# Performance work log

Hardware: AMD Instinct MI355X
Metric: run time of the kernel (lower is better)

## Reference

```python
import jax, jax.numpy as jnp
import numpy as np

C, C_LO, C_MF = 96, 32, 32  # c_hf = 96 - 32 - 32 = 32
K_LO, K_HI, LP_FINE, LP_COARSE = 5, 3, 3, 7
BN_EPS = 1e-5


def _avgpool_same(x, k):
    """AvgPool2d(k, stride=1, padding=k//2, count_include_pad=False) on NCHW."""
    p = k // 2
    dims, strides = (1, 1, k, k), (1, 1, 1, 1)
    pads = ((0, 0), (0, 0), (p, p), (p, p))
    s = jax.lax.reduce_window(x, jnp.float32(0), jax.lax.add, dims, strides, pads)
    ones = jnp.ones((1, 1) + x.shape[2:], x.dtype)
    cnt = jax.lax.reduce_window(ones, jnp.float32(0), jax.lax.add, dims, strides, pads)
    return s / cnt  # divide by number of VALID (non-pad) elements


def _dwconv(x, w, k):
    """Depthwise conv, 'same' padding, no bias. w: (C, 1, k, k)."""
    p = k // 2
    return jax.lax.conv_general_dilated(
        x, w, window_strides=(1, 1), padding=((p, p), (p, p)),
        dimension_numbers=("NCHW", "OIHW", "NCHW"),
        feature_group_count=x.shape[1])


def setup_inputs() -> dict:
    key = jax.random.key(0)
    ks = jax.random.split(key, 8)
    B, H, W = 8, 256, 256
    return {
        "x": jax.random.normal(ks[0], (B, C, H, W), jnp.float32),
        "w_lo": jax.random.normal(ks[1], (C_LO, 1, K_LO, K_LO), jnp.float32) * 0.1,
        "w_mf": jax.random.normal(ks[2], (C_MF, 1, 3, 3), jnp.float32) * 0.2,
        "w_hf": jax.random.normal(ks[3], (C - C_LO - C_MF, 1, K_HI, K_HI), jnp.float32) * 0.2,
        "bn_gamma": jax.random.uniform(ks[4], (C,), jnp.float32, 0.5, 1.5),
        "bn_beta": jax.random.normal(ks[5], (C,), jnp.float32) * 0.1,
        "bn_mean": jax.random.normal(ks[6], (C,), jnp.float32) * 0.1,
        "bn_var": jax.random.uniform(ks[7], (C,), jnp.float32, 0.5, 1.5),
    }


def reference(x, w_lo, w_mf, w_hf, bn_gamma, bn_beta, bn_mean, bn_var):
    x_lo = x[:, :C_LO]
    x_mf = x[:, C_LO:C_LO + C_MF]
    x_hf = x[:, C_LO + C_MF:]

    y_lo = _dwconv(x_lo, w_lo, K_LO)
    # band-pass: fine low-pass minus coarse low-pass
    x_mf_bp = _avgpool_same(x_mf, LP_FINE) - _avgpool_same(x_mf, LP_COARSE)
    y_mf = _dwconv(x_mf_bp, w_mf, 3)
    # high-pass: identity minus fine low-pass
    x_hf_hp = x_hf - _avgpool_same(x_hf, LP_FINE)
    y_hf = _dwconv(x_hf_hp, w_hf, K_HI)

    y = jnp.concatenate([y_lo, y_mf, y_hf], axis=1)

    # channel shuffle with groups=3 (C % 3 == 0 here)
    B, Cc, H, W = y.shape
    y = y.reshape(B, 3, Cc // 3, H, W).transpose(0, 2, 1, 3, 4).reshape(B, Cc, H, W)

    # BatchNorm2d (inference mode, running stats) + SiLU
    inv = bn_gamma * jax.lax.rsqrt(bn_var + BN_EPS)
    y = y * inv[None, :, None, None] + (bn_beta - bn_mean * inv)[None, :, None, None]
    return jax.nn.silu(y)
```

## Files before the change

kernel.cpp:

```cpp
#include <hip/hip_runtime.h>

#define HH 256
#define WW 256
#define CC 96
#define BB 8

__device__ __forceinline__ float silu_of(float z) {
    return z / (1.0f + __expf(-z));
}

__global__ __launch_bounds__(256, 4)
void trifreq_kernel(const float* __restrict__ x,
                    const float* __restrict__ w_lo,
                    const float* __restrict__ w_mf,
                    const float* __restrict__ w_hf,
                    const float* __restrict__ gamma,
                    const float* __restrict__ beta,
                    const float* __restrict__ mean,
                    const float* __restrict__ var,
                    float* __restrict__ out)
{
    __shared__ float xs[72 * 72];
    __shared__ float tmp[68 * 68];

    const int tid = threadIdx.x;
    const int tileIdx = blockIdx.x;
    const int c = blockIdx.y;
    const int b = blockIdx.z;
    const int th = (tileIdx >> 2) * 64;
    const int tw = (tileIdx & 3) * 64;

    const int g = c >> 5;
    const int ci = c & 31;
    const int c_out = ci * 3 + g;

    const float* __restrict__ xin = x + (((size_t)b * CC + c) * (size_t)HH) * (size_t)WW;

    for (int idx = tid; idx < 72 * 18; idx += 256) {
        const int r  = idx / 18;
        const int c4 = idx % 18;
        const int gh = th - 4 + r;
        const int gw = tw - 4 + 4 * c4;
        float4 v = make_float4(0.f, 0.f, 0.f, 0.f);
        if (gh >= 0 && gh < HH && gw >= 0 && gw + 3 < WW) {
            v = *reinterpret_cast<const float4*>(xin + (size_t)gh * WW + gw);
        }
        *reinterpret_cast<float4*>(&xs[r * 72 + 4 * c4]) = v;
    }
    __syncthreads();

    const int qr = (tid >> 4) << 2;
    const int qc = (tid & 15) << 2;
    float acc[4][4];

    if (g == 0) {
        const float* __restrict__ wp = w_lo + ci * 25;
        float wk[25];
        #pragma unroll
        for (int t = 0; t < 25; ++t) wk[t] = wp[t];
        #pragma unroll
        for (int i = 0; i < 4; ++i)
            #pragma unroll
            for (int j = 0; j < 4; ++j) acc[i][j] = 0.f;

        #pragma unroll
        for (int rr = 0; rr < 8; ++rr) {
            const float* row = &xs[(qr + rr + 2) * 72 + (qc + 2)];
            float v[8];
            #pragma unroll
            for (int j = 0; j < 8; ++j) v[j] = row[j];
            #pragma unroll
            for (int i = 0; i < 4; ++i) {
                const int ki = rr - i;
                if (ki >= 0 && ki < 5) {
                    #pragma unroll
                    for (int j = 0; j < 4; ++j)
                        acc[i][j] += v[j + 0] * wk[ki * 5 + 0]
                                   + v[j + 1] * wk[ki * 5 + 1]
                                   + v[j + 2] * wk[ki * 5 + 2]
                                   + v[j + 3] * wk[ki * 5 + 3]
                                   + v[j + 4] * wk[ki * 5 + 4];
                }
            }
        }
    } else {
        if (g == 1) {
            for (int p = tid; p < 17 * 17; p += 256) {
                const int pr = p / 17, pc = p % 17;
                const int br = pr * 4 - 2, bc = pc * 4 - 2;
                float v7a[4][4] = {};
                float v3a[4][4] = {};
                #pragma unroll
                for (int rr = 0; rr < 10; ++rr) {
                    int xr = br - 3 + rr + 4;
                    xr = max(0, min(71, xr));
                    const float* row = &xs[xr * 72];
                    float v[10];
                    #pragma unroll
                    for (int j = 0; j < 10; ++j) {
                        int xc = bc - 3 + j + 4;
                        xc = max(0, min(71, xc));
                        v[j] = row[xc];
                    }
                    float h7[4], h3[4];
                    float s = v[0] + v[1] + v[2] + v[3] + v[4] + v[5] + v[6];
                    h7[0] = s;
                    h7[1] = h7[0] + v[7] - v[0];
                    h7[2] = h7[1] + v[8] - v[1];
                    h7[3] = h7[2] + v[9] - v[2];
                    #pragma unroll
                    for (int j = 0; j < 4; ++j) h3[j] = v[j + 2] + v[j + 3] + v[j + 4];
                    #pragma unroll
                    for (int k = 0; k < 4; ++k) {
                        if (rr >= k && rr <= k + 6) {
                            #pragma unroll
                            for (int j = 0; j < 4; ++j) v7a[k][j] += h7[j];
                        }
                        if (rr >= k + 2 && rr <= k + 4) {
                            #pragma unroll
                            for (int j = 0; j < 4; ++j) v3a[k][j] += h3[j];
                        }
                    }
                }
                float r3h[4], r7h[4], r3w[4], r7w[4];
                #pragma unroll
                for (int i = 0; i < 4; ++i) {
                    const int hh = th + br + i;
                    const int a3 = min(hh + 1, HH - 1) - max(hh - 1, 0) + 1;
                    const int a7 = min(hh + 3, HH - 1) - max(hh - 3, 0) + 1;
                    r3h[i] = 1.0f / (float)a3;
                    r7h[i] = 1.0f / (float)a7;
                }
                #pragma unroll
                for (int j = 0; j < 4; ++j) {
                    const int ww = tw + bc + j;
                    const int a3 = min(ww + 1, WW - 1) - max(ww - 1, 0) + 1;
                    const int a7 = min(ww + 3, WW - 1) - max(ww - 3, 0) + 1;
                    r3w[j] = 1.0f / (float)a3;
                    r7w[j] = 1.0f / (float)a7;
                }
                #pragma unroll
                for (int i = 0; i < 4; ++i) {
                    const int hh = th + br + i;
                    #pragma unroll
                    for (int j = 0; j < 4; ++j) {
                        const int ww = tw + bc + j;
                        float bp = 0.f;
                        if (hh >= 0 && hh < HH && ww >= 0 && ww < WW)
                            bp = v3a[i][j] * (r3h[i] * r3w[j]) - v7a[i][j] * (r7h[i] * r7w[j]);
                        tmp[(br + i + 2) * 68 + (bc + j + 2)] = bp;
                    }
                }
            }
        } else {
            for (int p = tid; p < 17 * 17; p += 256) {
                const int pr = p / 17, pc = p % 17;
                const int br = pr * 4 - 2, bc = pc * 4 - 2;
                float v3a[4][4] = {};
                float cen[4][4];
                #pragma unroll
                for (int rr = 0; rr < 6; ++rr) {
                    const int xr = br - 1 + rr + 4;
                    const float* row = &xs[xr * 72];
                    float v[6];
                    #pragma unroll
                    for (int j = 0; j < 6; ++j) v[j] = row[bc - 1 + j + 4];
                    float h3[4];
                    #pragma unroll
                    for (int j = 0; j < 4; ++j) h3[j] = v[j] + v[j + 1] + v[j + 2];
                    if (rr >= 1 && rr <= 4) {
                        #pragma unroll
                        for (int j = 0; j < 4; ++j) cen[rr - 1][j] = v[j + 1];
                    }
                    #pragma unroll
                    for (int k = 0; k < 4; ++k) {
                        if (rr >= k && rr <= k + 2) {
                            #pragma unroll
                            for (int j = 0; j < 4; ++j) v3a[k][j] += h3[j];
                        }
                    }
                }
                float r3h[4], r3w[4];
                #pragma unroll
                for (int i = 0; i < 4; ++i) {
                    const int hh = th + br + i;
                    const int a3 = min(hh + 1, HH - 1) - max(hh - 1, 0) + 1;
                    r3h[i] = 1.0f / (float)a3;
                }
                #pragma unroll
                for (int j = 0; j < 4; ++j) {
                    const int ww = tw + bc + j;
                    const int a3 = min(ww + 1, WW - 1) - max(ww - 1, 0) + 1;
                    r3w[j] = 1.0f / (float)a3;
                }
                #pragma unroll
                for (int i = 0; i < 4; ++i) {
                    const int hh = th + br + i;
                    #pragma unroll
                    for (int j = 0; j < 4; ++j) {
                        const int ww = tw + bc + j;
                        float hp = 0.f;
                        if (hh >= 0 && hh < HH && ww >= 0 && ww < WW)
                            hp = cen[i][j] - v3a[i][j] * (r3h[i] * r3w[j]);
                        tmp[(br + i + 2) * 68 + (bc + j + 2)] = hp;
                    }
                }
            }
        }
        __syncthreads();

        const float* __restrict__ wp = ((g == 1) ? w_mf : w_hf) + ci * 9;
        float wk[9];
        #pragma unroll
        for (int t = 0; t < 9; ++t) wk[t] = wp[t];
        #pragma unroll
        for (int i = 0; i < 4; ++i)
            #pragma unroll
            for (int j = 0; j < 4; ++j) acc[i][j] = 0.f;

        #pragma unroll
        for (int rr = 0; rr < 6; ++rr) {
            const float* row = &tmp[(qr + rr + 1) * 68 + (qc + 1)];
            float v[6];
            #pragma unroll
            for (int j = 0; j < 6; ++j) v[j] = row[j];
            #pragma unroll
            for (int i = 0; i < 4; ++i) {
                const int ki = rr - i;
                if (ki >= 0 && ki < 3) {
                    #pragma unroll
                    for (int j = 0; j < 4; ++j)
                        acc[i][j] += v[j + 0] * wk[ki * 3 + 0]
                                   + v[j + 1] * wk[ki * 3 + 1]
                                   + v[j + 2] * wk[ki * 3 + 2];
                }
            }
        }
    }

    const float bninv  = gamma[c_out] * rsqrtf(var[c_out] + 1e-5f);
    const float bnbias = beta[c_out] - mean[c_out] * bninv;
    float* __restrict__ op = out + (((size_t)b * CC + c_out) * (size_t)HH + (th + qr)) * (size_t)WW + (tw + qc);
    #pragma unroll
    for (int i = 0; i < 4; ++i) {
        float4 o;
        const float z0 = acc[i][0] * bninv + bnbias;
        const float z1 = acc[i][1] * bninv + bnbias;
        const float z2 = acc[i][2] * bninv + bnbias;
        const float z3 = acc[i][3] * bninv + bnbias;
        o.x = silu_of(z0);
        o.y = silu_of(z1);
        o.z = silu_of(z2);
        o.w = silu_of(z3);
        *reinterpret_cast<float4*>(op + (size_t)i * WW) = o;
    }
}

extern "C" void kernel_launch(void* const* d_in, const int* in_sizes, int n_in,
                              void* d_out, int out_size, void* d_ws, size_t ws_size,
                              hipStream_t stream) {
    const float* x     = (const float*)d_in[0];
    const float* w_lo  = (const float*)d_in[1];
    const float* w_mf  = (const float*)d_in[2];
    const float* w_hf  = (const float*)d_in[3];
    const float* gam   = (const float*)d_in[4];
    const float* bet   = (const float*)d_in[5];
    const float* mea   = (const float*)d_in[6];
    const float* va    = (const float*)d_in[7];
    float* out = (float*)d_out;

    dim3 grid(16, CC, BB);
    dim3 block(256);
    hipLaunchKernelGGL(trifreq_kernel, grid, block, 0, stream,
                       x, w_lo, w_mf, w_hf, gam, bet, mea, va, out);
}
```

Measured before the change: 390.3 us.

## Use separable shared-memory box filters with smaller 32x64 tiles and precomputed reciprocals

Splits the avgpool filters into a horizontal running-sum pass stored in shared memory, followed by a vertical float4 sum pass. This replaces the per-thread 4x4 recomputation with clamped indexing. Tiles shrink to 32x64, doubling the grid and giving each thread a 2x4 output block. Valid-count reciprocals are precomputed once per block into a small table. This trades more halo overhead and extra barriers for less redundant ALU work, and the higher block count should help occupancy.

Result: no change. 393.4 us (+0.8%).

```diff
diff --git a/kernel.cpp b/kernel.cpp
--- a/kernel.cpp
+++ b/kernel.cpp
@@ -4,6 +4,13 @@
 #define WW 256
 #define CC 96
 #define BB 8
+
+#define TLH 32
+#define TLW 64
+#define XSH 40
+#define XSW 72
+#define HSH 40
+#define HSW 68
 
 __device__ __forceinline__ float silu_of(float z) {
     return z / (1.0f + __expf(-z));
@@ -20,38 +27,49 @@
                     const float* __restrict__ var,
                     float* __restrict__ out)
 {
-    __shared__ float xs[72 * 72];
-    __shared__ float tmp[68 * 68];
+    __shared__ __align__(16) float xs[XSH * XSW];
+    __shared__ __align__(16) float hsA[HSH * HSW];
+    __shared__ __align__(16) float hs7[HSH * HSW];
+    __shared__ float rc[4 * HSW];
 
     const int tid = threadIdx.x;
     const int tileIdx = blockIdx.x;
     const int c = blockIdx.y;
     const int b = blockIdx.z;
-    const int th = (tileIdx >> 2) * 64;
-    const int tw = (tileIdx & 3) * 64;
-
-    const int g = c >> 5;
+    const int th = (tileIdx >> 2) * TLH;
+    const int tw = (tileIdx & 3) * TLW;
+
+    const int g  = c >> 5;
     const int ci = c & 31;
     const int c_out = ci * 3 + g;
 
-    const float* __restrict__ xin = x + (((size_t)b * CC + c) * (size_t)HH) * (size_t)WW;
-
-    for (int idx = tid; idx < 72 * 18; idx += 256) {
+    const float* __restrict__ xin = x + (size_t)(b * CC + c) * (size_t)(HH * WW);
+
+    for (int i = tid; i < 4 * HSW; i += 256) {
+        const int tbl = i / HSW;
+        const int k   = i - tbl * HSW;
+        const int pos = ((tbl < 2) ? th : tw) + (k - 1);
+        const int rad = (tbl & 1) ? 3 : 1;
+        const int cnt = min(pos + rad, HH - 1) - max(pos - rad, 0) + 1;
+        rc[i] = (pos >= 0 && pos < HH) ? (1.0f / (float)cnt) : 0.0f;
+    }
+
+    for (int idx = tid; idx < XSH * 18; idx += 256) {
         const int r  = idx / 18;
-        const int c4 = idx % 18;
+        const int c4 = (idx - r * 18) * 4;
         const int gh = th - 4 + r;
-        const int gw = tw - 4 + 4 * c4;
+        const int gw = tw - 4 + c4;
         float4 v = make_float4(0.f, 0.f, 0.f, 0.f);
-        if (gh >= 0 && gh < HH && gw >= 0 && gw + 3 < WW) {
+        if ((unsigned)gh < (unsigned)HH && (unsigned)gw <= (unsigned)(WW - 4))
             v = *reinterpret_cast<const float4*>(xin + (size_t)gh * WW + gw);
-        }
-        *reinterpret_cast<float4*>(&xs[r * 72 + 4 * c4]) = v;
+        *reinterpret_cast<float4*>(&xs[r * XSW + c4]) = v;
     }
     __syncthreads();
 
-    const int qr = (tid >> 4) << 2;
-    const int qc = (tid & 15) << 2;
-    float acc[4][4];
+    const int qr = (tid >> 4) * 2;
+    const int qc = (tid & 15) * 4;
+    float acc0[4] = {0.f, 0.f, 0.f, 0.f};
+    float acc1[4] = {0.f, 0.f, 0.f, 0.f};
 
     if (g == 0) {
         const float* __restrict__ wp = w_lo + ci * 25;
@@ -59,152 +77,97 @@
         #pragma unroll
         for (int t = 0; t < 25; ++t) wk[t] = wp[t];
         #pragma unroll
-        for (int i = 0; i < 4; ++i)
-            #pragma unroll
-            for (int j = 0; j < 4; ++j) acc[i][j] = 0.f;
-
-        #pragma unroll
-        for (int rr = 0; rr < 8; ++rr) {
-            const float* row = &xs[(qr + rr + 2) * 72 + (qc + 2)];
+        for (int rr = 0; rr < 6; ++rr) {
+            const float* row = &xs[(qr + rr + 2) * XSW + (qc + 2)];
             float v[8];
             #pragma unroll
             for (int j = 0; j < 8; ++j) v[j] = row[j];
-            #pragma unroll
-            for (int i = 0; i < 4; ++i) {
-                const int ki = rr - i;
-                if (ki >= 0 && ki < 5) {
-                    #pragma unroll
-                    for (int j = 0; j < 4; ++j)
-                        acc[i][j] += v[j + 0] * wk[ki * 5 + 0]
-                                   + v[j + 1] * wk[ki * 5 + 1]
-                                   + v[j + 2] * wk[ki * 5 + 2]
-                                   + v[j + 3] * wk[ki * 5 + 3]
-                                   + v[j + 4] * wk[ki * 5 + 4];
+            if (rr < 5) {
+                const float* wr = &wk[rr * 5];
+                #pragma unroll
+                for (int j = 0; j < 4; ++j)
+                    acc0[j] += v[j]*wr[0] + v[j+1]*wr[1] + v[j+2]*wr[2] + v[j+3]*wr[3] + v[j+4]*wr[4];
+            }
+            if (rr >= 1) {
+                const float* wr = &wk[(rr - 1) * 5];
+                #pragma unroll
+                for (int j = 0; j < 4; ++j)
+                    acc1[j] += v[j]*wr[0] + v[j+1]*wr[1] + v[j+2]*wr[2] + v[j+3]*wr[3] + v[j+4]*wr[4];
+            }
+        }
+    } else {
+        for (int t = tid; t < HSH * 11; t += 256) {
+            const int r   = t / 11;
+            const int ci0 = (t - r * 11) * 6;
+            const float* row = &xs[r * XSW + ci0];
+            float v[12];
+            #pragma unroll
+            for (int j = 0; j < 12; ++j) v[j] = row[j];
+            float s7 = v[0]+v[1]+v[2]+v[3]+v[4]+v[5]+v[6];
+            float s3 = v[2]+v[3]+v[4];
+            float* p7 = &hs7[r * HSW + ci0];
+            float* p3 = &hsA[r * HSW + ci0];
+            #pragma unroll
+            for (int j = 0; j < 6; ++j) {
+                p7[j] = s7;
+                p3[j] = s3;
+                if (j < 5) { s7 += v[j+7] - v[j]; s3 += v[j+5] - v[j+2]; }
+            }
+        }
+        __syncthreads();
+
+        float res[3][4];
+        if (g == 1) {
+            int nt = 0;
+            for (int t = tid; t < 34 * 17; t += 256, ++nt) {
+                const int r   = t / 17;
+                const int ci0 = (t - r * 17) * 4;
+                float a7x=0.f, a7y=0.f, a7z=0.f, a7w=0.f;
+                #pragma unroll
+                for (int d = 0; d < 7; ++d) {
+                    const float4 h = *reinterpret_cast<const float4*>(&hs7[(r + d) * HSW + ci0]);
+                    a7x += h.x; a7y += h.y; a7z += h.z; a7w += h.w;
                 }
-            }
-        }
-    } else {
-        if (g == 1) {
-            for (int p = tid; p < 17 * 17; p += 256) {
-                const int pr = p / 17, pc = p % 17;
-                const int br = pr * 4 - 2, bc = pc * 4 - 2;
-                float v7a[4][4] = {};
-                float v3a[4][4] = {};
-                #pragma unroll
-                for (int rr = 0; rr < 10; ++rr) {
-                    int xr = br - 3 + rr + 4;
-                    xr = max(0, min(71, xr));
-                    const float* row = &xs[xr * 72];
-                    float v[10];
-                    #pragma unroll
-                    for (int j = 0; j < 10; ++j) {
-                        int xc = bc - 3 + j + 4;
-                        xc = max(0, min(71, xc));
-                        v[j] = row[xc];
-                    }
-                    float h7[4], h3[4];
-                    float s = v[0] + v[1] + v[2] + v[3] + v[4] + v[5] + v[6];
-                    h7[0] = s;
-                    h7[1] = h7[0] + v[7] - v[0];
-                    h7[2] = h7[1] + v[8] - v[1];
-                    h7[3] = h7[2] + v[9] - v[2];
-                    #pragma unroll
-                    for (int j = 0; j < 4; ++j) h3[j] = v[j + 2] + v[j + 3] + v[j + 4];
-                    #pragma unroll
-                    for (int k = 0; k < 4; ++k) {
-                        if (rr >= k && rr <= k + 6) {
-                            #pragma unroll
-                            for (int j = 0; j < 4; ++j) v7a[k][j] += h7[j];
-                        }
-                        if (rr >= k + 2 && rr <= k + 4) {
-                            #pragma unroll
-                            for (int j = 0; j < 4; ++j) v3a[k][j] += h3[j];
-                        }
-                    }
+                float a3x=0.f, a3y=0.f, a3z=0.f, a3w=0.f;
+                #pragma unroll
+                for (int d = 2; d < 5; ++d) {
+                    const float4 h = *reinterpret_cast<const float4*>(&hsA[(r + d) * HSW + ci0]);
+                    a3x += h.x; a3y += h.y; a3z += h.z; a3w += h.w;
                 }
-                float r3h[4], r7h[4], r3w[4], r7w[4];
-                #pragma unroll
-                for (int i = 0; i < 4; ++i) {
-                    const int hh = th + br + i;
-                    const int a3 = min(hh + 1, HH - 1) - max(hh - 1, 0) + 1;
-                    const int a7 = min(hh + 3, HH - 1) - max(hh - 3, 0) + 1;
-                    r3h[i] = 1.0f / (float)a3;
-                    r7h[i] = 1.0f / (float)a7;
+                const float f3 = rc[r];
+                const float f7 = rc[HSW + r];
+                res[nt][0] = a3x * (f3 * rc[2*HSW + ci0 + 0]) - a7x * (f7 * rc[3*HSW + ci0 + 0]);
+                res[nt][1] = a3y * (f3 * rc[2*HSW + ci0 + 1]) - a7y * (f7 * rc[3*HSW + ci0 + 1]);
+                res[nt][2] = a3z * (f3 * rc[2*HSW + ci0 + 2]) - a7z * (f7 * rc[3*HSW + ci0 + 2]);
+                res[nt][3] = a3w * (f3 * rc[2*HSW + ci0 + 3]) - a7w * (f7 * rc[3*HSW + ci0 + 3]);
+            }
+        } else {
+            int nt = 0;
+            for (int t = tid; t < 34 * 17; t += 256, ++nt) {
+                const int r   = t / 17;
+                const int ci0 = (t - r * 17) * 4;
+                float a3x=0.f, a3y=0.f, a3z=0.f, a3w=0.f;
+                #pragma unroll
+                for (int d = 2; d < 5; ++d) {
+                    const float4 h = *reinterpret_cast<const float4*>(&hsA[(r + d) * HSW + ci0]);
+                    a3x += h.x; a3y += h.y; a3z += h.z; a3w += h.w;
                 }
-                #pragma unroll
-                for (int j = 0; j < 4; ++j) {
-                    const int ww = tw + bc + j;
-                    const int a3 = min(ww + 1, WW - 1) - max(ww - 1, 0) + 1;
-                    const int a7 = min(ww + 3, WW - 1) - max(ww - 3, 0) + 1;
-                    r3w[j] = 1.0f / (float)a3;
-                    r7w[j] = 1.0f / (float)a7;
-                }
-                #pragma unroll
-                for (int i = 0; i < 4; ++i) {
-                    const int hh = th + br + i;
-                    #pragma unroll
-                    for (int j = 0; j < 4; ++j) {
-                        const int ww = tw + bc + j;
-                        float bp = 0.f;
-                        if (hh >= 0 && hh < HH && ww >= 0 && ww < WW)
-                            bp = v3a[i][j] * (r3h[i] * r3w[j]) - v7a[i][j] * (r7h[i] * r7w[j]);
-                        tmp[(br + i + 2) * 68 + (bc + j + 2)] = bp;
-                    }
-                }
-            }
-        } else {
-            for (int p = tid; p < 17 * 17; p += 256) {
-                const int pr = p / 17, pc = p % 17;
-                const int br = pr * 4 - 2, bc = pc * 4 - 2;
-                float v3a[4][4] = {};
-                float cen[4][4];
-                #pragma unroll
-                for (int rr = 0; rr < 6; ++rr) {
-                    const int xr = br - 1 + rr + 4;
-                    const float* row = &xs[xr * 72];
-                    float v[6];
-                    #pragma unroll
-                    for (int j = 0; j < 6; ++j) v[j] = row[bc - 1 + j + 4];
-                    float h3[4];
-                    #pragma unroll
-                    for (int j = 0; j < 4; ++j) h3[j] = v[j] + v[j + 1] + v[j + 2];
-                    if (rr >= 1 && rr <= 4) {
-                        #pragma unroll
-                        for (int j = 0; j < 4; ++j) cen[rr - 1][j] = v[j + 1];
-                    }
-                    #pragma unroll
-                    for (int k = 0; k < 4; ++k) {
-                        if (rr >= k && rr <= k + 2) {
-                            #pragma unroll
-                            for (int j = 0; j < 4; ++j) v3a[k][j] += h3[j];
-                        }
-                    }
-                }
-                float r3h[4], r3w[4];
-                #pragma unroll
-                for (int i = 0; i < 4; ++i) {
-                    const int hh = th + br + i;
-                    const int a3 = min(hh + 1, HH - 1) - max(hh - 1, 0) + 1;
-                    r3h[i] = 1.0f / (float)a3;
-                }
-                #pragma unroll
-                for (int j = 0; j < 4; ++j) {
-                    const int ww = tw + bc + j;
-                    const int a3 = min(ww + 1, WW - 1) - max(ww - 1, 0) + 1;
-                    r3w[j] = 1.0f / (float)a3;
-                }
-                #pragma unroll
-                for (int i = 0; i < 4; ++i) {
-                    const int hh = th + br + i;
-                    #pragma unroll
-                    for (int j = 0; j < 4; ++j) {
-                        const int ww = tw + bc + j;
-                        float hp = 0.f;
-                        if (hh >= 0 && hh < HH && ww >= 0 && ww < WW)
-                            hp = cen[i][j] - v3a[i][j] * (r3h[i] * r3w[j]);
-                        tmp[(br + i + 2) * 68 + (bc + j + 2)] = hp;
-                    }
-                }
+                const float f3 = rc[r];
+                const float* xr = &xs[(r + 3) * XSW + (ci0 + 3)];
+                res[nt][0] = xr[0] - a3x * (f3 * rc[2*HSW + ci0 + 0]);
+                res[nt][1] = xr[1] - a3y * (f3 * rc[2*HSW + ci0 + 1]);
+                res[nt][2] = xr[2] - a3z * (f3 * rc[2*HSW + ci0 + 2]);
+                res[nt][3] = xr[3] - a3w * (f3 * rc[2*HSW + ci0 + 3]);
+            }
+        }
+        __syncthreads();
+        {
+            int nt = 0;
+            for (int t = tid; t < 34 * 17; t += 256, ++nt) {
+                const int r   = t / 17;
+                const int ci0 = (t - r * 17) * 4;
+                *reinterpret_cast<float4*>(&hsA[r * HSW + ci0]) =
+                    make_float4(res[nt][0], res[nt][1], res[nt][2], res[nt][3]);
             }
         }
         __syncthreads();
@@ -214,62 +177,56 @@
         #pragma unroll
         for (int t = 0; t < 9; ++t) wk[t] = wp[t];
         #pragma unroll
-        for (int i = 0; i < 4; ++i)
-            #pragma unroll
-            for (int j = 0; j < 4; ++j) acc[i][j] = 0.f;
-
-        #pragma unroll
-        for (int rr = 0; rr < 6; ++rr) {
-            const float* row = &tmp[(qr + rr + 1) * 68 + (qc + 1)];
+        for (int rr = 0; rr < 4; ++rr) {
+            const float* row = &hsA[(qr + rr) * HSW + qc];
             float v[6];
             #pragma unroll
             for (int j = 0; j < 6; ++j) v[j] = row[j];
-            #pragma unroll
-            for (int i = 0; i < 4; ++i) {
-                const int ki = rr - i;
-                if (ki >= 0 && ki < 3) {
-                    #pragma unroll
-                    for (int j = 0; j < 4; ++j)
-                        acc[i][j] += v[j + 0] * wk[ki * 3 + 0]
-                                   + v[j + 1] * wk[ki * 3 + 1]
-                                   + v[j + 2] * wk[ki * 3 + 2];
-                }
+            if (rr < 3) {
+                const float* wr = &wk[rr * 3];
+                #pragma unroll
+                for (int j = 0; j < 4; ++j)
+                    acc0[j] += v[j]*wr[0] + v[j+1]*wr[1] + v[j+2]*wr[2];
+            }
+            if (rr >= 1) {
+                const float* wr = &wk[(rr - 1) * 3];
+                #pragma unroll
+                for (int j = 0; j < 4; ++j)
+                    acc1[j] += v[j]*wr[0] + v[j+1]*wr[1] + v[j+2]*wr[2];
             }
         }
     }
 
     const float bninv  = gamma[c_out] * rsqrtf(var[c_out] + 1e-5f);
     const float bnbias = beta[c_out] - mean[c_out] * bninv;
-    float* __restrict__ op = out + (((size_t)b * CC + c_out) * (size_t)HH + (th + qr)) * (size_t)WW + (tw + qc);
-    #pragma unroll
-    for (int i = 0; i < 4; ++i) {
-        float4 o;
-        const float z0 = acc[i][0] * bninv + bnbias;
-        const float z1 = acc[i][1] * bninv + bnbias;
-        const float z2 = acc[i][2] * bninv + bnbias;
-        const float z3 = acc[i][3] * bninv + bnbias;
-        o.x = silu_of(z0);
-        o.y = silu_of(z1);
-        o.z = silu_of(z2);
-        o.w = silu_of(z3);
-        *reinterpret_cast<float4*>(op + (size_t)i * WW) = o;
-    }
+    float* __restrict__ op = out + ((size_t)(b * CC + c_out) * HH + (th + qr)) * (size_t)WW + (tw + qc);
+    float4 o0, o1;
+    o0.x = silu_of(acc0[0] * bninv + bnbias);
+    o0.y = silu_of(acc0[1] * bninv + bnbias);
+    o0.z = silu_of(acc0[2] * bninv + bnbias);
+    o0.w = silu_of(acc0[3] * bninv + bnbias);
+    o1.x = silu_of(acc1[0] * bninv + bnbias);
+    o1.y = silu_of(acc1[1] * bninv + bnbias);
+    o1.z = silu_of(acc1[2] * bninv + bnbias);
+    o1.w = silu_of(acc1[3] * bninv + bnbias);
+    *reinterpret_cast<float4*>(op) = o0;
+    *reinterpret_cast<float4*>(op + WW) = o1;
 }
 
 extern "C" void kernel_launch(void* const* d_in, const int* in_sizes, int n_in,
                               void* d_out, int out_size, void* d_ws, size_t ws_size,
                               hipStream_t stream) {
-    const float* x     = (const float*)d_in[0];
-    const float* w_lo  = (const float*)d_in[1];
-    const float* w_mf  = (const float*)d_in[2];
-    const float* w_hf  = (const float*)d_in[3];
-    const float* gam   = (const float*)d_in[4];
-    const float* bet   = (const float*)d_in[5];
-    const float* mea   = (const float*)d_in[6];
-    const float* va    = (const float*)d_in[7];
+    const float* x    = (const float*)d_in[0];
+    const float* w_lo = (const float*)d_in[1];
+    const float* w_mf = (const float*)d_in[2];
+    const float* w_hf = (const float*)d_in[3];
+    const float* gam  = (const float*)d_in[4];
+    const float* bet  = (const float*)d_in[5];
+    const float* mea  = (const float*)d_in[6];
+    const float* va   = (const float*)d_in[7];
     float* out = (float*)d_out;
 
-    dim3 grid(16, CC, BB);
+    dim3 grid(32, CC, BB);
     dim3 block(256);
     hipLaunchKernelGGL(trifreq_kernel, grid, block, 0, stream,
                        x, w_lo, w_mf, w_hf, gam, bet, mea, va, out);
```
